# Optimization experiments

Measured on AMD Instinct MI355X. Metric: run time of the kernel, lower is better.

## Reference

```python
import jax, jax.numpy as jnp
import numpy as np

L, NK = 4, 6  # num blocks, Nk geodesic components

def _gelu(x):
    return jax.nn.gelu(x, approximate=False)  # torch nn.GELU default (erf)

def _ln(x, g, b, eps=1e-5):
    m = jnp.mean(x, axis=-1, keepdims=True)
    v = jnp.mean((x - m) ** 2, axis=-1, keepdims=True)
    return (x - m) * jax.lax.rsqrt(v + eps) * g + b


def setup_inputs() -> dict:
    B, N, C, M = 4, 8192, 64, 64
    key = jax.random.key(0)
    ks = iter(jax.random.split(key, 48))
    def nrm(*s):
        return jax.random.normal(next(ks), s, dtype=jnp.float32) * 0.02
    inp = {
        'x': jax.random.normal(next(ks), (B, N, 1), dtype=jnp.float32),
        'MATRIX_Phy': jax.random.normal(next(ks), (N, M), dtype=jnp.float32) * 0.02,
        'INVERSE_Phy': jax.random.normal(next(ks), (M, N), dtype=jnp.float32) * 0.02,
        'meshPoints': jax.random.normal(next(ks), (N, 3), dtype=jnp.float32),
        'adj_norm': jax.random.uniform(next(ks), (N, N), dtype=jnp.float32) / N,
    }
    inp.update(
        fc0_w=nrm(4, C), fc0_b=jnp.zeros(C), fc01_w=nrm(C, C), fc01_b=jnp.zeros(C),
        blk_ln1_g=jnp.ones((L, C)), blk_ln1_b=jnp.zeros((L, C)),
        norm1_g=jnp.ones((L, C)), norm1_b=jnp.zeros((L, C)),
        spec_w=jax.random.uniform(next(ks), (L, NK, C, C, M), dtype=jnp.float32) / (C * C),
        enc_p1_w=nrm(L, 3, C), enc_p1_b=jnp.zeros((L, C)),
        enc_p2_w=nrm(L, C, C), enc_p2_b=jnp.zeros((L, C)),
        enc_g1_w=nrm(L, C, C), enc_g1_b=jnp.zeros((L, C)),
        enc_g2_w=nrm(L, C, C), enc_g2_b=jnp.zeros((L, C)),
        enc_o1_w=nrm(L, C, 2 * C), enc_o1_b=jnp.zeros((L, 2 * C)),
        enc_o2_w=nrm(L, 2 * C, NK), enc_o2_b=jnp.zeros((L, NK)),
        spat_g1_w=nrm(L, C, 2 * C), spat_g1_b=jnp.zeros((L, 2 * C)),
        spat_g2_w=nrm(L, 2 * C, C), spat_g2_b=jnp.zeros((L, C)),
        blk_ln2_g=jnp.ones((L, C)), blk_ln2_b=jnp.zeros((L, C)),
        mlp_pre_w=nrm(L, C, 2 * C), mlp_pre_b=jnp.zeros((L, 2 * C)),
        mlp_post_w=nrm(L, 2 * C, C), mlp_post_b=jnp.zeros((L, C)),
        ln1_g=jnp.ones(C), ln1_b=jnp.zeros(C),
        fc1_w=nrm(C, 128), fc1_b=jnp.zeros(128),
        fc2_w=nrm(128, 1), fc2_b=jnp.zeros(1),
    )
    return inp


def reference(x, MATRIX_Phy, INVERSE_Phy, meshPoints, adj_norm,
              fc0_w, fc0_b, fc01_w, fc01_b,
              blk_ln1_g, blk_ln1_b, norm1_g, norm1_b, spec_w,
              enc_p1_w, enc_p1_b, enc_p2_w, enc_p2_b,
              enc_g1_w, enc_g1_b, enc_g2_w, enc_g2_b,
              enc_o1_w, enc_o1_b, enc_o2_w, enc_o2_b,
              spat_g1_w, spat_g1_b, spat_g2_w, spat_g2_b,
              blk_ln2_g, blk_ln2_b, mlp_pre_w, mlp_pre_b, mlp_post_w, mlp_post_b,
              ln1_g, ln1_b, fc1_w, fc1_b, fc2_w, fc2_b):
    B = x.shape[0]
    mesh = jnp.broadcast_to(meshPoints[None], (B,) + meshPoints.shape)  # [B,N,3]
    h = jnp.concatenate([x, mesh], axis=-1)                             # [B,N,4]
    h = h @ fc0_w + fc0_b
    h = h @ fc01_w + fc01_b                                             # [B,N,C]
    for l in range(L):
        z = _ln(h, blk_ln1_g[l], blk_ln1_b[l])
        # --- MeshGCN encoder -> geodesic mixing coefficients geoT [M,Nk] ---
        e = _gelu(meshPoints @ enc_p1_w[l] + enc_p1_b[l]) @ enc_p2_w[l] + enc_p2_b[l]
        e = _gelu(adj_norm @ (e @ enc_g1_w[l] + enc_g1_b[l]))
        e = adj_norm @ (e @ enc_g2_w[l] + enc_g2_b[l])
        e = (e @ enc_o1_w[l] + enc_o1_b[l]) @ enc_o2_w[l] + enc_o2_b[l]  # [N,Nk]
        geoT = jax.nn.softmax(INVERSE_Phy @ e, axis=1)                   # [M,Nk]
        # --- geodesic-modulated spectral conv ---
        cm = jnp.einsum('mn,bnc->bcm', INVERSE_Phy, z)                   # [B,C,M]
        w = jnp.einsum('kiom,mk->iom', spec_w[l], geoT)                  # [C,C,M]
        cg = jnp.einsum('bim,iom->bom', cm, w)                           # [B,C,M]
        x1 = jnp.einsum('bom,nm->bno', cg, MATRIX_Phy)                   # [B,N,C]
        x1 = _ln(x1, norm1_g[l], norm1_b[l])
        # --- spatial GCN branch (SimpleGCN: gcn->relu->gcn) ---
        s = jax.nn.relu(jnp.einsum('mn,bnc->bmc', adj_norm, z @ spat_g1_w[l] + spat_g1_b[l]))
        x2 = jnp.einsum('mn,bnc->bmc', adj_norm, s @ spat_g2_w[l] + spat_g2_b[l])
        h = x1 + x2 + h
        z2 = _ln(h, blk_ln2_g[l], blk_ln2_b[l])
        h = _gelu(z2 @ mlp_pre_w[l] + mlp_pre_b[l]) @ mlp_post_w[l] + mlp_post_b[l] + h
    h = _gelu(_ln(h, ln1_g, ln1_b) @ fc1_w + fc1_b)
    return h @ fc2_w + fc2_b                                             # [B,N,1]
```

## Files before the change

kernel.cpp:

```cpp
#include <hip/hip_runtime.h>
#include <math.h>

typedef __bf16 bf16_t;
typedef __bf16 bf16x8 __attribute__((ext_vector_type(8)));
typedef __bf16 bf16x4 __attribute__((ext_vector_type(4)));
typedef float  f32x4  __attribute__((ext_vector_type(4)));

#define NN 8192
#define RA 8320
#define GP1F 2129920
#define XPAD 68
#define X2PAD 132
#define ZTPAD 66

__device__ __forceinline__ float gelu_f(float x) {
    return 0.5f * x * (1.0f + erff(x * 0.70710678118654752f));
}

__device__ __forceinline__ float wsum64(float v) {
#pragma unroll
    for (int m = 32; m; m >>= 1) v += __shfl_xor(v, m);
    return v;
}

__device__ __forceinline__ float gp4(const float* __restrict__ Gp, size_t gi) {
    return (Gp[gi] + Gp[gi + (size_t)GP1F]) + (Gp[gi + 2 * (size_t)GP1F] + Gp[gi + 3 * (size_t)GP1F]);
}

__device__ __forceinline__ void async16(const void* g, void* l) {
    __builtin_amdgcn_global_load_lds(
        (const __attribute__((address_space(1))) unsigned int*)g,
        (__attribute__((address_space(3))) unsigned int*)l,
        16, 0, 0);
}

__device__ __forceinline__ void mm16(const float* __restrict__ X, int xpad,
                                     const float* __restrict__ W, int ws, int K,
                                     int c, int r0, float* acc) {
    for (int k0 = 0; k0 < K; k0 += 4) {
        float w0 = W[(size_t)(k0 + 0) * ws + c];
        float w1 = W[(size_t)(k0 + 1) * ws + c];
        float w2 = W[(size_t)(k0 + 2) * ws + c];
        float w3 = W[(size_t)(k0 + 3) * ws + c];
#pragma unroll
        for (int i = 0; i < 16; ++i) {
            float4 xv = *(const float4*)(X + (size_t)(r0 + i) * xpad + k0);
            acc[i] = fmaf(xv.x, w0, acc[i]);
            acc[i] = fmaf(xv.y, w1, acc[i]);
            acc[i] = fmaf(xv.z, w2, acc[i]);
            acc[i] = fmaf(xv.w, w3, acc[i]);
        }
    }
}

__global__ __launch_bounds__(256) void k_adj_convert(const float* __restrict__ adj,
                                                     const float* __restrict__ INV,
                                                     bf16_t* __restrict__ adjB,
                                                     float* __restrict__ rowsum) {
    int row = blockIdx.x;
    int t = threadIdx.x;
    bf16_t* br = adjB + (size_t)row * NN;
    if (row >= NN + 64) {
        bf16x4 zz; zz[0] = zz[1] = zz[2] = zz[3] = (bf16_t)0.f;
#pragma unroll
        for (int v = 0; v < 8; ++v) *(bf16x4*)(br + (v * 256 + t) * 4) = zz;
        return;
    }
    const float* ar = (row < NN) ? adj + (size_t)row * NN : INV + (size_t)(row - NN) * NN;
    float s = 0.f;
#pragma unroll
    for (int v = 0; v < 8; ++v) {
        int i = (v * 256 + t) * 4;
        float4 f = *(const float4*)(ar + i);
        s += f.x + f.y + f.z + f.w;
        bf16x4 o;
        o[0] = (bf16_t)f.x; o[1] = (bf16_t)f.y; o[2] = (bf16_t)f.z; o[3] = (bf16_t)f.w;
        *(bf16x4*)(br + i) = o;
    }
    if (row < NN) {
        s = wsum64(s);
        __shared__ float w4[4];
        if ((t & 63) == 0) w4[t >> 6] = s;
        __syncthreads();
        if (t == 0) rowsum[row] = w4[0] + w4[1] + w4[2] + w4[3];
    }
}

__global__ __launch_bounds__(64) void k_fold(const float* __restrict__ fc0w, const float* __restrict__ fc0b,
                                             const float* __restrict__ fc01w, const float* __restrict__ fc01b,
                                             float* __restrict__ W0b) {
    int c = threadIdx.x;
#pragma unroll
    for (int j = 0; j < 4; ++j) {
        float a = 0.f;
        for (int k = 0; k < 64; ++k) a += fc0w[j * 64 + k] * fc01w[k * 64 + c];
        W0b[j * 64 + c] = a;
    }
    float b = fc01b[c];
    for (int k = 0; k < 64; ++k) b += fc0b[k] * fc01w[k * 64 + c];
    W0b[256 + c] = b;
}

__global__ __launch_bounds__(256) void k_init_h(const float* __restrict__ x, const float* __restrict__ mesh,
                         const float* __restrict__ W0b,
                         const float* __restrict__ zg, const float* __restrict__ zb,
                         float* __restrict__ h, bf16_t* __restrict__ Vt) {
    __shared__ __align__(16) char buf[64 * ZTPAD * 2];
    bf16_t* ZT = (bf16_t*)buf;
    int t = threadIdx.x, c = t & 63, rq = t >> 6, r0 = rq * 16;
    int bb = blockIdx.x >> 7, n0 = (blockIdx.x & 127) * 64;
    float w0c = W0b[c], w1c = W0b[64 + c], w2c = W0b[128 + c], w3c = W0b[192 + c], b0c = W0b[256 + c];
    float gc = zg[c], bc = zb[c];
#pragma unroll
    for (int q = 0; q < 16; ++q) {
        int n = n0 + r0 + q;
        int w = bb * NN + n;
        float xv = x[w];
        float m0 = mesh[n * 3], m1 = mesh[n * 3 + 1], m2 = mesh[n * 3 + 2];
        float hv = b0c + xv * w0c + m0 * w1c + m1 * w2c + m2 * w3c;
        h[(size_t)w * 64 + c] = hv;
        float s = wsum64(hv), s2 = wsum64(hv * hv);
        float mean = s * (1.f / 64.f), var = s2 * (1.f / 64.f) - mean * mean;
        float z = (hv - mean) * rsqrtf(var + 1e-5f) * gc + bc;
        ZT[c * ZTPAD + r0 + q] = (bf16_t)z;
    }
    __syncthreads();
#pragma unroll
    for (int cc = 0; cc < 16; ++cc) {
        int c2 = r0 + cc;
        Vt[(size_t)(bb * 64 + c2) * NN + n0 + c] = ZT[c2 * ZTPAD + c];
    }
}

__global__ __launch_bounds__(256) void k_enc_pre(const float* __restrict__ mesh,
                          const float* __restrict__ p1w, const float* __restrict__ p1b,
                          const float* __restrict__ p2w, const float* __restrict__ p2b,
                          const float* __restrict__ g1w, const float* __restrict__ g1b,
                          bf16_t* __restrict__ Vt) {
    __shared__ __align__(16) char buf[2 * 64 * XPAD * 4];
    float* X1 = (float*)buf;
    float* X2 = (float*)(buf + 64 * XPAD * 4);
    bf16_t* ZT = (bf16_t*)buf;
    int t = threadIdx.x, c = t & 63, rq = t >> 6, r0 = rq * 16;
    int ll = blockIdx.x >> 7, n0 = (blockIdx.x & 127) * 64;
    float p1b_c = p1b[ll * 64 + c];
    float p1w0 = p1w[(ll * 3 + 0) * 64 + c], p1w1 = p1w[(ll * 3 + 1) * 64 + c], p1w2 = p1w[(ll * 3 + 2) * 64 + c];
#pragma unroll
    for (int q = 0; q < 16; ++q) {
        int n = n0 + r0 + q;
        float m0 = mesh[n * 3], m1 = mesh[n * 3 + 1], m2 = mesh[n * 3 + 2];
        X1[(r0 + q) * XPAD + c] = gelu_f(p1b_c + m0 * p1w0 + m1 * p1w1 + m2 * p1w2);
    }
    __syncthreads();
    float e2[16];
#pragma unroll
    for (int i = 0; i < 16; ++i) e2[i] = p2b[ll * 64 + c];
    mm16(X1, XPAD, p2w + ll * 4096, 64, 64, c, r0, e2);
    __syncthreads();
#pragma unroll
    for (int q = 0; q < 16; ++q) X2[(r0 + q) * XPAD + c] = e2[q];
    __syncthreads();
    float tt[16];
#pragma unroll
    for (int i = 0; i < 16; ++i) tt[i] = g1b[ll * 64 + c];
    mm16(X2, XPAD, g1w + ll * 4096, 64, 64, c, r0, tt);
#pragma unroll
    for (int q = 0; q < 16; ++q) ZT[c * ZTPAD + r0 + q] = (bf16_t)tt[q];
    __syncthreads();
#pragma unroll
    for (int cc = 0; cc < 16; ++cc) {
        int c2 = r0 + cc;
        Vt[(size_t)(ll * 64 + c2) * NN + n0 + c] = ZT[c2 * ZTPAD + c];
    }
}

__global__ __launch_bounds__(256) void k_enc_mid(const float* __restrict__ Gp,
                          const float* __restrict__ g2w, const float* __restrict__ g2b,
                          bf16_t* __restrict__ Vt) {
    __shared__ __align__(16) char buf[64 * XPAD * 4 + 64 * ZTPAD * 2];
    float* X = (float*)buf;
    bf16_t* ZT = (bf16_t*)(buf + 64 * XPAD * 4);
    int t = threadIdx.x, c = t & 63, rq = t >> 6, r0 = rq * 16;
    int ll = blockIdx.x >> 7, n0 = (blockIdx.x & 127) * 64;
#pragma unroll
    for (int q = 0; q < 16; ++q) {
        int n = n0 + r0 + q;
        X[(r0 + q) * XPAD + c] = gelu_f(gp4(Gp, (size_t)n * 256 + ll * 64 + c));
    }
    __syncthreads();
    float t2[16];
#pragma unroll
    for (int i = 0; i < 16; ++i) t2[i] = g2b[ll * 64 + c];
    mm16(X, XPAD, g2w + ll * 4096, 64, 64, c, r0, t2);
#pragma unroll
    for (int q = 0; q < 16; ++q) ZT[c * ZTPAD + r0 + q] = (bf16_t)t2[q];
    __syncthreads();
#pragma unroll
    for (int cc = 0; cc < 16; ++cc) {
        int c2 = r0 + cc;
        Vt[(size_t)(ll * 64 + c2) * NN + n0 + c] = ZT[c2 * ZTPAD + c];
    }
}

__global__ void k_geo_part(const float* __restrict__ Gp,
                           const float* __restrict__ o1w, const float* __restrict__ o1b,
                           const float* __restrict__ o2w, const float* __restrict__ o2b,
                           const float* __restrict__ INV,
                           float* __restrict__ partials) {
    int l = blockIdx.x >> 7, chunk = blockIdx.x & 127;
    int n0 = chunk * 64;
    int t = threadIdx.x;
    __shared__ float e4L[64][65];
    for (int r = 0; r < 64; ++r) {
        size_t gi = (size_t)(n0 + r) * 256 + l * 64 + t;
        e4L[r][t] = gp4(Gp, gi);
    }
    __syncthreads();
    float X[64];
#pragma unroll
    for (int i = 0; i < 64; ++i) X[i] = e4L[t][i];
    float e5[6] = {0, 0, 0, 0, 0, 0};
    const float* o1wl = o1w + (size_t)l * 64 * 128;
    const float* o2wl = o2w + (size_t)l * 128 * 6;
    for (int j = 0; j < 128; ++j) {
        float a = o1b[l * 128 + j];
#pragma unroll
        for (int i = 0; i < 64; ++i) a += X[i] * o1wl[i * 128 + j];
#pragma unroll
        for (int k = 0; k < 6; ++k) e5[k] += a * o2wl[j * 6 + k];
    }
#pragma unroll
    for (int k = 0; k < 6; ++k) e5[k] += o2b[l * 6 + k];
    __shared__ float e5L[64][8];
#pragma unroll
    for (int k = 0; k < 6; ++k) e5L[t][k] = e5[k];
    __syncthreads();
    float p[6] = {0, 0, 0, 0, 0, 0};
    const float* ivr = INV + (size_t)t * NN + n0;
    for (int r = 0; r < 64; ++r) {
        float iv = ivr[r];
#pragma unroll
        for (int k = 0; k < 6; ++k) p[k] += iv * e5L[r][k];
    }
#pragma unroll
    for (int k = 0; k < 6; ++k) partials[(size_t)(((l * 128 + chunk) * 64) + t) * 6 + k] = p[k];
}

__global__ void k_geo_final(const float* __restrict__ partials, float* __restrict__ geoT) {
    int l = blockIdx.x, m = threadIdx.x;
    float g[6] = {0, 0, 0, 0, 0, 0};
    for (int ch = 0; ch < 128; ++ch) {
#pragma unroll
        for (int k = 0; k < 6; ++k) g[k] += partials[(size_t)(((l * 128 + ch) * 64) + m) * 6 + k];
    }
    float mx = g[0];
#pragma unroll
    for (int k = 1; k < 6; ++k) mx = fmaxf(mx, g[k]);
    float s = 0.f;
#pragma unroll
    for (int k = 0; k < 6; ++k) { g[k] = expf(g[k] - mx); s += g[k]; }
    float inv = 1.f / s;
#pragma unroll
    for (int k = 0; k < 6; ++k) geoT[(size_t)(l * 64 + m) * 6 + k] = g[k] * inv;
}

__global__ __launch_bounds__(64) void k_w(const float* __restrict__ specw,
                                          const float* __restrict__ geoT,
                                          float* __restrict__ wAll) {
    int l = blockIdx.x >> 12, io = blockIdx.x & 4095;
    int m = threadIdx.x;
    float a = 0.f;
#pragma unroll
    for (int k = 0; k < 6; ++k)
        a += specw[(((size_t)l * 6 + k) * 4096 + io) * 64 + m] * geoT[(size_t)(l * 64 + m) * 6 + k];
    wAll[((size_t)l * 4096 + io) * 64 + m] = a;
}

__global__ __launch_bounds__(256) void k_cmsum(const float* __restrict__ Gp, float* __restrict__ cmc) {
    int bi = blockIdx.x * 4 + (threadIdx.x >> 6);
    int m = threadIdx.x & 63;
    size_t gi = (size_t)(NN + m) * 256 + bi;
    cmc[bi * 64 + m] = gp4(Gp, gi);
}

__global__ __launch_bounds__(256) void k_cg2(const float* __restrict__ cmc,
                                             const float* __restrict__ wl,
                                             float* __restrict__ cgT) {
    int o = blockIdx.x;
    int b = threadIdx.x >> 6, m = threadIdx.x & 63;
    float acc = 0.f;
    for (int i = 0; i < 64; ++i)
        acc += cmc[(b * 64 + i) * 64 + m] * wl[((size_t)(i * 64 + o)) * 64 + m];
    cgT[(b * 64 + m) * 64 + o] = acc;
}

__global__ __launch_bounds__(256) void k_spat_mid(const float* __restrict__ Gp,
                           const float* __restrict__ W1, const float* __restrict__ b1,
                           const float* __restrict__ W2, const float* __restrict__ b2,
                           const float* __restrict__ rowsum, bf16_t* __restrict__ Vt) {
    __shared__ __align__(16) char buf[64 * XPAD * 4 + 64 * X2PAD * 4];
    float* X  = (float*)buf;
    float* X2 = (float*)(buf + 64 * XPAD * 4);
    bf16_t* ZT = (bf16_t*)buf;
    int t = threadIdx.x, c = t & 63, rq = t >> 6, r0 = rq * 16;
    int bb = blockIdx.x >> 7, n0 = (blockIdx.x & 127) * 64;
    float rs[16];
#pragma unroll
    for (int q = 0; q < 16; ++q) {
        int m = n0 + r0 + q;
        rs[q] = rowsum[m];
        X[(r0 + q) * XPAD + c] = gp4(Gp, (size_t)m * 256 + bb * 64 + c);
    }
    __syncthreads();
    float ma0[16], ma1[16];
    float b1c0 = b1[c], b1c1 = b1[64 + c];
#pragma unroll
    for (int i = 0; i < 16; ++i) { ma0[i] = rs[i] * b1c0; ma1[i] = rs[i] * b1c1; }
    mm16(X, XPAD, W1, 128, 64, c, r0, ma0);
    mm16(X, XPAD, W1 + 64, 128, 64, c, r0, ma1);
    __syncthreads();
#pragma unroll
    for (int q = 0; q < 16; ++q) {
        X2[(r0 + q) * X2PAD + c] = fmaxf(ma0[q], 0.f);
        X2[(r0 + q) * X2PAD + 64 + c] = fmaxf(ma1[q], 0.f);
    }
    __syncthreads();
    float y[16];
#pragma unroll
    for (int i = 0; i < 16; ++i) y[i] = b2[c];
    mm16(X2, X2PAD, W2, 64, 128, c, r0, y);
#pragma unroll
    for (int q = 0; q < 16; ++q) ZT[c * ZTPAD + r0 + q] = (bf16_t)y[q];
    __syncthreads();
#pragma unroll
    for (int cc = 0; cc < 16; ++cc) {
        int c2 = r0 + cc;
        Vt[(size_t)(bb * 64 + c2) * NN + n0 + c] = ZT[c2 * ZTPAD + c];
    }
}

__global__ __launch_bounds__(256) void k_blk_post(float* __restrict__ h, const float* __restrict__ Gp,
                           const float* __restrict__ cgT, const float* __restrict__ MP,
                           const float* __restrict__ n1g, const float* __restrict__ n1b,
                           const float* __restrict__ l2g, const float* __restrict__ l2b,
                           const float* __restrict__ prew, const float* __restrict__ preb,
                           const float* __restrict__ postw, const float* __restrict__ postb,
                           const float* __restrict__ zng, const float* __restrict__ znb,
                           bf16_t* __restrict__ Vt, int writeZ) {
    __shared__ __align__(16) char buf[64 * X2PAD * 4 + 64 * XPAD * 4];
    float* MProws = (float*)buf;
    float* X2     = (float*)buf;
    float* X      = (float*)(buf + 64 * X2PAD * 4);
    bf16_t* ZT    = (bf16_t*)(buf + 64 * X2PAD * 4);
    int t = threadIdx.x, c = t & 63, rq = t >> 6, r0 = rq * 16;
    int bb = blockIdx.x >> 7, n0 = (blockIdx.x & 127) * 64;
#pragma unroll
    for (int q = 0; q < 16; ++q)
        MProws[(r0 + q) * XPAD + c] = MP[(size_t)(n0 + r0 + q) * 64 + c];
    __syncthreads();
    float x1[16];
#pragma unroll
    for (int i = 0; i < 16; ++i) x1[i] = 0.f;
    mm16(MProws, XPAD, cgT + (size_t)bb * 4096, 64, 64, c, r0, x1);
    float hv[16];
    float n1gc = n1g[c], n1bc = n1b[c];
#pragma unroll
    for (int q = 0; q < 16; ++q) {
        float s = wsum64(x1[q]), s2 = wsum64(x1[q] * x1[q]);
        float mean = s * (1.f / 64.f), var = s2 * (1.f / 64.f) - mean * mean;
        float x1n = (x1[q] - mean) * rsqrtf(var + 1e-5f) * n1gc + n1bc;
        int n = n0 + r0 + q;
        size_t w = (size_t)bb * NN + n;
        hv[q] = x1n + gp4(Gp, (size_t)n * 256 + bb * 64 + c) + h[w * 64 + c];
    }
    float l2gc = l2g[c], l2bc = l2b[c];
#pragma unroll
    for (int q = 0; q < 16; ++q) {
        float s = wsum64(hv[q]), s2 = wsum64(hv[q] * hv[q]);
        float mean = s * (1.f / 64.f), var = s2 * (1.f / 64.f) - mean * mean;
        X[(r0 + q) * XPAD + c] = (hv[q] - mean) * rsqrtf(var + 1e-5f) * l2gc + l2bc;
    }
    __syncthreads();
    float ma0[16], ma1[16];
    float pb0 = preb[c], pb1 = preb[64 + c];
#pragma unroll
    for (int i = 0; i < 16; ++i) { ma0[i] = pb0; ma1[i] = pb1; }
    mm16(X, XPAD, prew, 128, 64, c, r0, ma0);
    mm16(X, XPAD, prew + 64, 128, 64, c, r0, ma1);
    __syncthreads();
#pragma unroll
    for (int q = 0; q < 16; ++q) {
        X2[(r0 + q) * X2PAD + c] = gelu_f(ma0[q]);
        X2[(r0 + q) * X2PAD + 64 + c] = gelu_f(ma1[q]);
    }
    __syncthreads();
    float o[16];
    float pob = postb[c];
#pragma unroll
    for (int i = 0; i < 16; ++i) o[i] = pob;
    mm16(X2, X2PAD, postw, 64, 128, c, r0, o);
#pragma unroll
    for (int q = 0; q < 16; ++q) {
        hv[q] += o[q];
        h[((size_t)bb * NN + n0 + r0 + q) * 64 + c] = hv[q];
    }
    if (writeZ) {
        float zgc = zng[c], zbc = znb[c];
#pragma unroll
        for (int q = 0; q < 16; ++q) {
            float s = wsum64(hv[q]), s2 = wsum64(hv[q] * hv[q]);
            float mean = s * (1.f / 64.f), var = s2 * (1.f / 64.f) - mean * mean;
            ZT[c * ZTPAD + r0 + q] = (bf16_t)((hv[q] - mean) * rsqrtf(var + 1e-5f) * zgc + zbc);
        }
        __syncthreads();
#pragma unroll
        for (int cc = 0; cc < 16; ++cc) {
            int c2 = r0 + cc;
            Vt[(size_t)(bb * 64 + c2) * NN + n0 + c] = ZT[c2 * ZTPAD + c];
        }
    }
}

__global__ __launch_bounds__(256) void k_head(const float* __restrict__ h,
                       const float* __restrict__ g, const float* __restrict__ bb_,
                       const float* __restrict__ fc1w, const float* __restrict__ fc1b,
                       const float* __restrict__ fc2w, const float* __restrict__ fc2b,
                       float* __restrict__ out) {
    __shared__ __align__(16) char buf[64 * XPAD * 4 + 64 * X2PAD * 4];
    float* X  = (float*)buf;
    float* X2 = (float*)(buf + 64 * XPAD * 4);
    int t = threadIdx.x, c = t & 63, rq = t >> 6, r0 = rq * 16;
    int bb = blockIdx.x >> 7, n0 = (blockIdx.x & 127) * 64;
    float gc = g[c], bc = bb_[c];
#pragma unroll
    for (int q = 0; q < 16; ++q) {
        float hv = h[((size_t)bb * NN + n0 + r0 + q) * 64 + c];
        float s = wsum64(hv), s2 = wsum64(hv * hv);
        float mean = s * (1.f / 64.f), var = s2 * (1.f / 64.f) - mean * mean;
        X[(r0 + q) * XPAD + c] = (hv - mean) * rsqrtf(var + 1e-5f) * gc + bc;
    }
    __syncthreads();
    float ma0[16], ma1[16];
    float fb0 = fc1b[c], fb1 = fc1b[64 + c];
#pragma unroll
    for (int i = 0; i < 16; ++i) { ma0[i] = fb0; ma1[i] = fb1; }
    mm16(X, XPAD, fc1w, 128, 64, c, r0, ma0);
    mm16(X, XPAD, fc1w + 64, 128, 64, c, r0, ma1);
    __syncthreads();
#pragma unroll
    for (int q = 0; q < 16; ++q) {
        X2[(r0 + q) * X2PAD + c] = gelu_f(ma0[q]);
        X2[(r0 + q) * X2PAD + 64 + c] = gelu_f(ma1[q]);
    }
    __syncthreads();
    float f2a = fc2w[c], f2b = fc2w[64 + c], f2bias = fc2b[0];
#pragma unroll
    for (int q = 0; q < 16; ++q) {
        float val = X2[(r0 + q) * X2PAD + c] * f2a + X2[(r0 + q) * X2PAD + 64 + c] * f2b;
        val = wsum64(val);
        if (c == 0) out[(size_t)bb * NN + n0 + r0 + q] = val + f2bias;
    }
}

__global__ __launch_bounds__(256) void gemm_bf16(const bf16_t* __restrict__ A,
                                                 const bf16_t* __restrict__ Bt,
                                                 float* __restrict__ Gp) {
    __shared__ __align__(16) char smem[2][24576];
    const int bid = blockIdx.x;
    const int tile = (bid & 7) * 130 + (bid >> 3);
    const int ks = tile / 260;
    const int r2 = tile % 260;
    const int tn = r2 & 3;
    const int tm = r2 >> 2;
    const int kt0 = ks * 32;
    const int nkt = 32;

    const int t = threadIdx.x;
    const int lane = t & 63, wid = t >> 6;
    const int wr = wid >> 1, wc = wid & 1;
    const int lrow = lane & 15, lk = lane >> 4;

    const bf16_t* Abase = A + (size_t)tm * 128 * NN;
    const bf16_t* Bbase = Bt + (size_t)tn * 64 * NN;

    f32x4 acc[4][2];
#pragma unroll
    for (int i = 0; i < 4; ++i) {
        acc[i][0] = f32x4{0.f, 0.f, 0.f, 0.f};
        acc[i][1] = f32x4{0.f, 0.f, 0.f, 0.f};
    }

    auto stage = [&](int bsel, int kt) {
        char* lb = smem[bsel];
        int k0 = kt * 64;
#pragma unroll
        for (int r = 0; r < 4; ++r) {
            int ci = t + r * 256;
            int rw = ci >> 3, ch = ci & 7;
            int sch = ch ^ (rw & 7);
            async16(Abase + (size_t)rw * NN + k0 + sch * 8, lb + ci * 16);
        }
#pragma unroll
        for (int r = 0; r < 2; ++r) {
            int ci = t + r * 256;
            int rw = ci >> 3, ch = ci & 7;
            int sch = ch ^ (rw & 7);
            async16(Bbase + (size_t)rw * NN + k0 + sch * 8, lb + 16384 + ci * 16);
        }
    };

    stage(0, kt0);
    __syncthreads();
    for (int it = 0; it < nkt; ++it) {
        int cur = it & 1;
        if (it + 1 < nkt) stage(cur ^ 1, kt0 + it + 1);
        const char* lb = smem[cur];
#pragma unroll
        for (int kk = 0; kk < 2; ++kk) {
            bf16x8 av[4], bv[2];
#pragma unroll
            for (int i = 0; i < 4; ++i) {
                int R = wr * 64 + i * 16 + lrow;
                av[i] = *(const bf16x8*)(lb + R * 128 + (((kk * 4 + lk) ^ (R & 7)) << 4));
            }
#pragma unroll
            for (int j = 0; j < 2; ++j) {
                int Q = wc * 32 + j * 16 + lrow;
                bv[j] = *(const bf16x8*)(lb + 16384 + Q * 128 + (((kk * 4 + lk) ^ (Q & 7)) << 4));
            }
#pragma unroll
            for (int i = 0; i < 4; ++i)
#pragma unroll
                for (int j = 0; j < 2; ++j)
                    acc[i][j] = __builtin_amdgcn_mfma_f32_16x16x32_bf16(av[i], bv[j], acc[i][j], 0, 0, 0);
        }
        __syncthreads();
    }

    float* Cs = Gp + (size_t)ks * GP1F;
    int row0 = tm * 128 + wr * 64;
    int col0 = tn * 64 + wc * 32;
#pragma unroll
    for (int i = 0; i < 4; ++i)
#pragma unroll
        for (int j = 0; j < 2; ++j)
#pragma unroll
            for (int r = 0; r < 4; ++r)
                Cs[(size_t)(row0 + i * 16 + lk * 4 + r) * 256 + col0 + j * 16 + lrow] = acc[i][j][r];
}


extern "C" void kernel_launch(void* const* d_in, const int* in_sizes, int n_in,
                              void* d_out, int out_size, void* d_ws, size_t ws_size,
                              hipStream_t stream) {
    const float* x     = (const float*)d_in[0];
    const float* MP    = (const float*)d_in[1];
    const float* INV   = (const float*)d_in[2];
    const float* mesh  = (const float*)d_in[3];
    const float* adj   = (const float*)d_in[4];
    const float* fc0w  = (const float*)d_in[5];
    const float* fc0b  = (const float*)d_in[6];
    const float* fc01w = (const float*)d_in[7];
    const float* fc01b = (const float*)d_in[8];
    const float* bln1g = (const float*)d_in[9];
    const float* bln1b = (const float*)d_in[10];
    const float* n1g   = (const float*)d_in[11];
    const float* n1b   = (const float*)d_in[12];
    const float* specw = (const float*)d_in[13];
    const float* p1w   = (const float*)d_in[14];
    const float* p1b   = (const float*)d_in[15];
    const float* p2w   = (const float*)d_in[16];
    const float* p2b   = (const float*)d_in[17];
    const float* g1w   = (const float*)d_in[18];
    const float* g1b   = (const float*)d_in[19];
    const float* g2w   = (const float*)d_in[20];
    const float* g2b   = (const float*)d_in[21];
    const float* o1w   = (const float*)d_in[22];
    const float* o1b   = (const float*)d_in[23];
    const float* o2w   = (const float*)d_in[24];
    const float* o2b   = (const float*)d_in[25];
    const float* sg1w  = (const float*)d_in[26];
    const float* sg1b  = (const float*)d_in[27];
    const float* sg2w  = (const float*)d_in[28];
    const float* sg2b  = (const float*)d_in[29];
    const float* bln2g = (const float*)d_in[30];
    const float* bln2b = (const float*)d_in[31];
    const float* prew  = (const float*)d_in[32];
    const float* preb  = (const float*)d_in[33];
    const float* postw = (const float*)d_in[34];
    const float* postb = (const float*)d_in[35];
    const float* ln1g  = (const float*)d_in[36];
    const float* ln1b  = (const float*)d_in[37];
    const float* fc1w  = (const float*)d_in[38];
    const float* fc1b  = (const float*)d_in[39];
    const float* fc2w  = (const float*)d_in[40];
    const float* fc2b  = (const float*)d_in[41];
    float* out = (float*)d_out;

    char* ws = (char*)d_ws;
    bf16_t* adjB    = (bf16_t*)(ws);
    float*  Gp      = (float*) (ws + 136314880);
    bf16_t* Vt      = (bf16_t*)(ws + 170393600);
    float*  h       = (float*) (ws + 174587904);
    float*  rowsum  = (float*) (ws + 182976512);
    float*  partials= (float*) (ws + 183009280);
    float*  geoT    = (float*) (ws + 183795712);
    float*  wAll    = (float*) (ws + 183801856);
    float*  cmc     = (float*) (ws + 187996160);
    float*  cgT     = (float*) (ws + 188061696);
    float*  W0b     = (float*) (ws + 188127232);

    k_adj_convert<<<RA, 256, 0, stream>>>(adj, INV, adjB, rowsum);
    k_fold<<<1, 64, 0, stream>>>(fc0w, fc0b, fc01w, fc01b, W0b);

    k_enc_pre<<<512, 256, 0, stream>>>(mesh, p1w, p1b, p2w, p2b, g1w, g1b, Vt);
    gemm_bf16<<<1040, 256, 0, stream>>>(adjB, Vt, Gp);
    k_enc_mid<<<512, 256, 0, stream>>>(Gp, g2w, g2b, Vt);
    gemm_bf16<<<1040, 256, 0, stream>>>(adjB, Vt, Gp);
    k_geo_part<<<512, 64, 0, stream>>>(Gp, o1w, o1b, o2w, o2b, INV, partials);
    k_geo_final<<<4, 64, 0, stream>>>(partials, geoT);
    k_w<<<16384, 64, 0, stream>>>(specw, geoT, wAll);

    k_init_h<<<512, 256, 0, stream>>>(x, mesh, W0b, bln1g, bln1b, h, Vt);

    for (int l = 0; l < 4; ++l) {
        gemm_bf16<<<1040, 256, 0, stream>>>(adjB, Vt, Gp);
        k_cmsum<<<64, 256, 0, stream>>>(Gp, cmc);
        k_cg2<<<64, 256, 0, stream>>>(cmc, wAll + (size_t)l * 262144, cgT);
        k_spat_mid<<<512, 256, 0, stream>>>(Gp, sg1w + l * 64 * 128, sg1b + l * 128,
                                            sg2w + l * 128 * 64, sg2b + l * 64, rowsum, Vt);
        gemm_bf16<<<1040, 256, 0, stream>>>(adjB, Vt, Gp);
        int ln = (l < 3) ? (l + 1) : 3;
        k_blk_post<<<512, 256, 0, stream>>>(h, Gp, cgT, MP,
                                            n1g + l * 64, n1b + l * 64,
                                            bln2g + l * 64, bln2b + l * 64,
                                            prew + l * 64 * 128, preb + l * 128,
                                            postw + l * 128 * 64, postb + l * 64,
                                            bln1g + ln * 64, bln1b + ln * 64,
                                            Vt, (l < 3) ? 1 : 0);
    }

    k_head<<<512, 256, 0, stream>>>(h, ln1g, ln1b, fc1w, fc1b, fc2w, fc2b, out);
}
```

Measured before the change: 1.282 ms.

## Merge encoder and first block adjacency GEMMs and switch to 32x32 MFMA

The second encoder adjacency GEMM and the first block's adjacency GEMM are merged into one wider GEMM with 512 output columns, so the bf16 adjacency matrix is streamed once for both. The init-h kernel is moved earlier and writes its Vt into the upper 256 columns to make this possible. The GEMM kernel now takes a column-tile count and uses 32x32x16 MFMA instructions instead of 16x16x32. That gives fewer LDS fragment loads per MFMA but a different output store pattern. A separate 512-column partial buffer is added, which grows workspace use.

```diff
diff --git a/kernel.cpp b/kernel.cpp
--- a/kernel.cpp
+++ b/kernel.cpp
@@ -5,10 +5,12 @@
 typedef __bf16 bf16x8 __attribute__((ext_vector_type(8)));
 typedef __bf16 bf16x4 __attribute__((ext_vector_type(4)));
 typedef float  f32x4  __attribute__((ext_vector_type(4)));
+typedef float  f32x16 __attribute__((ext_vector_type(16)));
 
 #define NN 8192
 #define RA 8320
-#define GP1F 2129920
+#define GPS256 2129920u
+#define GPS512 4259840u
 #define XPAD 68
 #define X2PAD 132
 #define ZTPAD 66
@@ -23,8 +25,8 @@
     return v;
 }
 
-__device__ __forceinline__ float gp4(const float* __restrict__ Gp, size_t gi) {
-    return (Gp[gi] + Gp[gi + (size_t)GP1F]) + (Gp[gi + 2 * (size_t)GP1F] + Gp[gi + 3 * (size_t)GP1F]);
+__device__ __forceinline__ float gp4s(const float* __restrict__ Gp, size_t gi, size_t st) {
+    return (Gp[gi] + Gp[gi + st]) + (Gp[gi + 2 * st] + Gp[gi + 3 * st]);
 }
 
 __device__ __forceinline__ void async16(const void* g, void* l) {
@@ -128,7 +130,7 @@
 #pragma unroll
     for (int cc = 0; cc < 16; ++cc) {
         int c2 = r0 + cc;
-        Vt[(size_t)(bb * 64 + c2) * NN + n0 + c] = ZT[c2 * ZTPAD + c];
+        Vt[(size_t)(256 + bb * 64 + c2) * NN + n0 + c] = ZT[c2 * ZTPAD + c];
     }
 }
 
@@ -185,7 +187,7 @@
 #pragma unroll
     for (int q = 0; q < 16; ++q) {
         int n = n0 + r0 + q;
-        X[(r0 + q) * XPAD + c] = gelu_f(gp4(Gp, (size_t)n * 256 + ll * 64 + c));
+        X[(r0 + q) * XPAD + c] = gelu_f(gp4s(Gp, (size_t)n * 256 + ll * 64 + c, GPS256));
     }
     __syncthreads();
     float t2[16];
@@ -212,8 +214,8 @@
     int t = threadIdx.x;
     __shared__ float e4L[64][65];
     for (int r = 0; r < 64; ++r) {
-        size_t gi = (size_t)(n0 + r) * 256 + l * 64 + t;
-        e4L[r][t] = gp4(Gp, gi);
+        size_t gi = (size_t)(n0 + r) * 512 + l * 64 + t;
+        e4L[r][t] = gp4s(Gp, gi, GPS512);
     }
     __syncthreads();
     float X[64];
@@ -276,11 +278,13 @@
     wAll[((size_t)l * 4096 + io) * 64 + m] = a;
 }
 
-__global__ __launch_bounds__(256) void k_cmsum(const float* __restrict__ Gp, float* __restrict__ cmc) {
+__global__ __launch_bounds__(256) void k_cmsum(const float* __restrict__ Gp, float* __restrict__ cmc,
+                                               int ncols, int colbase) {
     int bi = blockIdx.x * 4 + (threadIdx.x >> 6);
     int m = threadIdx.x & 63;
-    size_t gi = (size_t)(NN + m) * 256 + bi;
-    cmc[bi * 64 + m] = gp4(Gp, gi);
+    size_t st = (size_t)RA * ncols;
+    size_t gi = (size_t)(NN + m) * ncols + colbase + bi;
+    cmc[bi * 64 + m] = gp4s(Gp, gi, st);
 }
 
 __global__ __launch_bounds__(256) void k_cg2(const float* __restrict__ cmc,
@@ -297,19 +301,21 @@
 __global__ __launch_bounds__(256) void k_spat_mid(const float* __restrict__ Gp,
                            const float* __restrict__ W1, const float* __restrict__ b1,
                            const float* __restrict__ W2, const float* __restrict__ b2,
-                           const float* __restrict__ rowsum, bf16_t* __restrict__ Vt) {
+                           const float* __restrict__ rowsum, bf16_t* __restrict__ Vt,
+                           int ncols, int colbase) {
     __shared__ __align__(16) char buf[64 * XPAD * 4 + 64 * X2PAD * 4];
     float* X  = (float*)buf;
     float* X2 = (float*)(buf + 64 * XPAD * 4);
     bf16_t* ZT = (bf16_t*)buf;
     int t = threadIdx.x, c = t & 63, rq = t >> 6, r0 = rq * 16;
     int bb = blockIdx.x >> 7, n0 = (blockIdx.x & 127) * 64;
+    size_t st = (size_t)RA * ncols;
     float rs[16];
 #pragma unroll
     for (int q = 0; q < 16; ++q) {
         int m = n0 + r0 + q;
         rs[q] = rowsum[m];
-        X[(r0 + q) * XPAD + c] = gp4(Gp, (size_t)m * 256 + bb * 64 + c);
+        X[(r0 + q) * XPAD + c] = gp4s(Gp, (size_t)m * ncols + colbase + bb * 64 + c, st);
     }
     __syncthreads();
     float ma0[16], ma1[16];
@@ -371,7 +377,7 @@
         float x1n = (x1[q] - mean) * rsqrtf(var + 1e-5f) * n1gc + n1bc;
         int n = n0 + r0 + q;
         size_t w = (size_t)bb * NN + n;
-        hv[q] = x1n + gp4(Gp, (size_t)n * 256 + bb * 64 + c) + h[w * 64 + c];
+        hv[q] = x1n + gp4s(Gp, (size_t)n * 256 + bb * 64 + c, GPS256) + h[w * 64 + c];
     }
     float l2gc = l2g[c], l2bc = l2b[c];
 #pragma unroll
@@ -416,7 +422,7 @@
 #pragma unroll
         for (int cc = 0; cc < 16; ++cc) {
             int c2 = r0 + cc;
-            Vt[(size_t)(bb * 64 + c2) * NN + n0 + c] = ZT[c2 * ZTPAD + c];
+            Vt[(size_t)(256 + bb * 64 + c2) * NN + n0 + c] = ZT[c2 * ZTPAD + c];
         }
     }
 }
@@ -464,31 +470,33 @@
 
 __global__ __launch_bounds__(256) void gemm_bf16(const bf16_t* __restrict__ A,
                                                  const bf16_t* __restrict__ Bt,
-                                                 float* __restrict__ Gp) {
+                                                 float* __restrict__ Gp,
+                                                 int ntn) {
     __shared__ __align__(16) char smem[2][24576];
+    const int cpx = gridDim.x >> 3;
     const int bid = blockIdx.x;
-    const int tile = (bid & 7) * 130 + (bid >> 3);
-    const int ks = tile / 260;
-    const int r2 = tile % 260;
-    const int tn = r2 & 3;
-    const int tm = r2 >> 2;
+    const int tile = (bid & 7) * cpx + (bid >> 3);
+    const unsigned pertile = 65u * (unsigned)ntn;
+    const int ks = (unsigned)tile / pertile;
+    const int r2 = (unsigned)tile % pertile;
+    const int tn = r2 & (ntn - 1);
+    const int tm = r2 / ntn;
     const int kt0 = ks * 32;
     const int nkt = 32;
+    const int ncols = ntn * 64;
 
     const int t = threadIdx.x;
     const int lane = t & 63, wid = t >> 6;
     const int wr = wid >> 1, wc = wid & 1;
-    const int lrow = lane & 15, lk = lane >> 4;
+    const int lm = lane & 31;
+    const int lkg = lane >> 5;
 
     const bf16_t* Abase = A + (size_t)tm * 128 * NN;
     const bf16_t* Bbase = Bt + (size_t)tn * 64 * NN;
 
-    f32x4 acc[4][2];
-#pragma unroll
-    for (int i = 0; i < 4; ++i) {
-        acc[i][0] = f32x4{0.f, 0.f, 0.f, 0.f};
-        acc[i][1] = f32x4{0.f, 0.f, 0.f, 0.f};
-    }
+    f32x16 acc0, acc1;
+#pragma unroll
+    for (int i = 0; i < 16; ++i) { acc0[i] = 0.f; acc1[i] = 0.f; }
 
     auto stage = [&](int bsel, int kt) {
         char* lb = smem[bsel];
@@ -509,6 +517,11 @@
         }
     };
 
+    const int R0 = wr * 64 + lm;
+    const int R1 = R0 + 32;
+    const int Q  = wc * 32 + lm;
+    const int swzA = R0 & 7, swzB = Q & 7;
+
     stage(0, kt0);
     __syncthreads();
     for (int it = 0; it < nkt; ++it) {
@@ -516,37 +529,30 @@
         if (it + 1 < nkt) stage(cur ^ 1, kt0 + it + 1);
         const char* lb = smem[cur];
 #pragma unroll
-        for (int kk = 0; kk < 2; ++kk) {
-            bf16x8 av[4], bv[2];
-#pragma unroll
-            for (int i = 0; i < 4; ++i) {
-                int R = wr * 64 + i * 16 + lrow;
-                av[i] = *(const bf16x8*)(lb + R * 128 + (((kk * 4 + lk) ^ (R & 7)) << 4));
-            }
-#pragma unroll
-            for (int j = 0; j < 2; ++j) {
-                int Q = wc * 32 + j * 16 + lrow;
-                bv[j] = *(const bf16x8*)(lb + 16384 + Q * 128 + (((kk * 4 + lk) ^ (Q & 7)) << 4));
-            }
-#pragma unroll
-            for (int i = 0; i < 4; ++i)
-#pragma unroll
-                for (int j = 0; j < 2; ++j)
-                    acc[i][j] = __builtin_amdgcn_mfma_f32_16x16x32_bf16(av[i], bv[j], acc[i][j], 0, 0, 0);
+        for (int ks4 = 0; ks4 < 4; ++ks4) {
+            int kc = ks4 * 2 + lkg;
+            bf16x8 av0 = *(const bf16x8*)(lb + R0 * 128 + ((kc ^ swzA) << 4));
+            bf16x8 av1 = *(const bf16x8*)(lb + R1 * 128 + ((kc ^ swzA) << 4));
+            bf16x8 bv  = *(const bf16x8*)(lb + 16384 + Q * 128 + ((kc ^ swzB) << 4));
+            acc0 = __builtin_amdgcn_mfma_f32_32x32x16_bf16(av0, bv, acc0, 0, 0, 0);
+            acc1 = __builtin_amdgcn_mfma_f32_32x32x16_bf16(av1, bv, acc1, 0, 0, 0);
         }
         __syncthreads();
     }
 
-    float* Cs = Gp + (size_t)ks * GP1F;
-    int row0 = tm * 128 + wr * 64;
-    int col0 = tn * 64 + wc * 32;
-#pragma unroll
-    for (int i = 0; i < 4; ++i)
-#pragma unroll
-        for (int j = 0; j < 2; ++j)
-#pragma unroll
-            for (int r = 0; r < 4; ++r)
-                Cs[(size_t)(row0 + i * 16 + lk * 4 + r) * 256 + col0 + j * 16 + lrow] = acc[i][j][r];
+    float* Cs = Gp + (size_t)ks * RA * ncols;
+    const int colg = tn * 64 + wc * 32 + lm;
+    const int rbase0 = tm * 128 + wr * 64 + 4 * lkg;
+#pragma unroll
+    for (int reg = 0; reg < 16; ++reg) {
+        int rrow = (reg & 3) + 8 * (reg >> 2);
+        Cs[(size_t)(rbase0 + rrow) * ncols + colg] = acc0[reg];
+    }
+#pragma unroll
+    for (int reg = 0; reg < 16; ++reg) {
+        int rrow = (reg & 3) + 8 * (reg >> 2);
+        Cs[(size_t)(rbase0 + 32 + rrow) * ncols + colg] = acc1[reg];
+    }
 }
 
 
@@ -599,39 +605,48 @@
 
     char* ws = (char*)d_ws;
     bf16_t* adjB    = (bf16_t*)(ws);
-    float*  Gp      = (float*) (ws + 136314880);
-    bf16_t* Vt      = (bf16_t*)(ws + 170393600);
-    float*  h       = (float*) (ws + 174587904);
-    float*  rowsum  = (float*) (ws + 182976512);
-    float*  partials= (float*) (ws + 183009280);
-    float*  geoT    = (float*) (ws + 183795712);
-    float*  wAll    = (float*) (ws + 183801856);
-    float*  cmc     = (float*) (ws + 187996160);
-    float*  cgT     = (float*) (ws + 188061696);
-    float*  W0b     = (float*) (ws + 188127232);
+    float*  Gp512   = (float*) (ws + 136314880);
+    float*  Gp256   = (float*) (ws + 204472320);
+    bf16_t* Vt      = (bf16_t*)(ws + 238551040);
+    float*  h       = (float*) (ws + 246939648);
+    float*  rowsum  = (float*) (ws + 255328256);
+    float*  partials= (float*) (ws + 255361024);
+    float*  geoT    = (float*) (ws + 256147456);
+    float*  wAll    = (float*) (ws + 256153600);
+    float*  cmc     = (float*) (ws + 260347904);
+    float*  cgT     = (float*) (ws + 260413440);
+    float*  W0b     = (float*) (ws + 260478976);
+
+    bf16_t* VtZ = Vt + (size_t)256 * NN;
 
     k_adj_convert<<<RA, 256, 0, stream>>>(adj, INV, adjB, rowsum);
     k_fold<<<1, 64, 0, stream>>>(fc0w, fc0b, fc01w, fc01b, W0b);
 
     k_enc_pre<<<512, 256, 0, stream>>>(mesh, p1w, p1b, p2w, p2b, g1w, g1b, Vt);
-    gemm_bf16<<<1040, 256, 0, stream>>>(adjB, Vt, Gp);
-    k_enc_mid<<<512, 256, 0, stream>>>(Gp, g2w, g2b, Vt);
-    gemm_bf16<<<1040, 256, 0, stream>>>(adjB, Vt, Gp);
-    k_geo_part<<<512, 64, 0, stream>>>(Gp, o1w, o1b, o2w, o2b, INV, partials);
+    gemm_bf16<<<1040, 256, 0, stream>>>(adjB, Vt, Gp256, 4);
+    k_enc_mid<<<512, 256, 0, stream>>>(Gp256, g2w, g2b, Vt);
+    k_init_h<<<512, 256, 0, stream>>>(x, mesh, W0b, bln1g, bln1b, h, Vt);
+
+    gemm_bf16<<<2080, 256, 0, stream>>>(adjB, Vt, Gp512, 8);
+
+    k_geo_part<<<512, 64, 0, stream>>>(Gp512, o1w, o1b, o2w, o2b, INV, partials);
     k_geo_final<<<4, 64, 0, stream>>>(partials, geoT);
     k_w<<<16384, 64, 0, stream>>>(specw, geoT, wAll);
 
-    k_init_h<<<512, 256, 0, stream>>>(x, mesh, W0b, bln1g, bln1b, h, Vt);
-
     for (int l = 0; l < 4; ++l) {
-        gemm_bf16<<<1040, 256, 0, stream>>>(adjB, Vt, Gp);
-        k_cmsum<<<64, 256, 0, stream>>>(Gp, cmc);
+        const float* Gp1 = Gp256; int nc = 256, cb = 0;
+        if (l == 0) { Gp1 = Gp512; nc = 512; cb = 256; }
+        else {
+            gemm_bf16<<<1040, 256, 0, stream>>>(adjB, VtZ, Gp256, 4);
+        }
+        k_cmsum<<<64, 256, 0, stream>>>(Gp1, cmc, nc, cb);
         k_cg2<<<64, 256, 0, stream>>>(cmc, wAll + (size_t)l * 262144, cgT);
-        k_spat_mid<<<512, 256, 0, stream>>>(Gp, sg1w + l * 64 * 128, sg1b + l * 128,
-                                            sg2w + l * 128 * 64, sg2b + l * 64, rowsum, Vt);
-        gemm_bf16<<<1040, 256, 0, stream>>>(adjB, Vt, Gp);
+        k_spat_mid<<<512, 256, 0, stream>>>(Gp1, sg1w + l * 64 * 128, sg1b + l * 128,
+                                            sg2w + l * 128 * 64, sg2b + l * 64, rowsum, Vt,
+                                            nc, cb);
+        gemm_bf16<<<1040, 256, 0, stream>>>(adjB, Vt, Gp256, 4);
         int ln = (l < 3) ? (l + 1) : 3;
-        k_blk_post<<<512, 256, 0, stream>>>(h, Gp, cgT, MP,
+        k_blk_post<<<512, 256, 0, stream>>>(h, Gp256, cgT, MP,
                                             n1g + l * 64, n1b + l * 64,
                                             bln2g + l * 64, bln2b + l * 64,
                                             prew + l * 64 * 128, preb + l * 128,
```

Result: no change. 1.294 ms (+1.0%).
